# Performance work log

Hardware: AMD Instinct MI355X
Metric: run time of the kernel (lower is better)

The kernel has to match this reference:

```python
import jax, jax.numpy as jnp
import numpy as np

C = 64
RED = 4            # attention reduction: conv_match C -> C//RED
CR = C // RED      # 16, also MultiScaleSpatialAttention reduced channels
N_HASHES = 4
CHUNK = 512
RES_SCALE = 0.1
EPS = 5e-5


def conv2d(x, w, b=None, padding=0, groups=1):
    out = jax.lax.conv_general_dilated(
        x, w, (1, 1), [(padding, padding), (padding, padding)],
        dimension_numbers=('NCHW', 'OIHW', 'NCHW'), feature_group_count=groups)
    if b is not None:
        out = out + b[None, :, None, None]
    return out


def ds_conv(x, pw_w, dw_w, dw_b, padding):
    # pointwise (no bias) then depthwise (bias)
    x = conv2d(x, pw_w)
    return conv2d(x, dw_w, dw_b, padding=padding, groups=dw_w.shape[0])


def pool2(x, mode):
    B, Cc, H, W = x.shape
    xr = x.reshape(B, Cc, H // 2, 2, W // 2, 2)
    return xr.max(axis=(3, 5)) if mode == 'max' else xr.mean(axis=(3, 5))


def bilinear_ac(x, out_h, out_w):
    # bilinear interpolation with align_corners=True (matches F.interpolate)
    B, Cc, h, w = x.shape
    def coords(n_in, n_out):
        pos = jnp.arange(n_out, dtype=x.dtype) * ((n_in - 1) / (n_out - 1))
        lo = jnp.floor(pos).astype(jnp.int32)
        hi = jnp.minimum(lo + 1, n_in - 1)
        frac = pos - lo.astype(x.dtype)
        return lo, hi, frac
    lo_h, hi_h, fh = coords(h, out_h)
    x = x[:, :, lo_h, :] * (1 - fh)[None, None, :, None] + x[:, :, hi_h, :] * fh[None, None, :, None]
    lo_w, hi_w, fw = coords(w, out_w)
    x = x[:, :, :, lo_w] * (1 - fw) + x[:, :, :, hi_w] * fw
    return x


def sparse_attn(x, wm, bm, wa, ba, rot):
    # NLSN-style LSH-chunked non-local sparse attention
    N, Cc, H, W = x.shape
    L = H * W
    xe = conv2d(x, wm, bm).reshape(N, -1, L).transpose(0, 2, 1)   # [N,L,Ce]
    ye = conv2d(x, wa, ba).reshape(N, -1, L).transpose(0, 2, 1)   # [N,L,C]
    Ce = xe.shape[-1]
    n_chunks = L // CHUNK                     # L multiple of CHUNK here -> no padding
    buckets = min(n_chunks + n_chunks % 2, 128)
    # LSH hashing (rot: [Ce, n_hashes, buckets//2])
    rv = jnp.einsum('blf,fhi->bhli', xe, rot)
    rv = jnp.concatenate([rv, -rv], axis=-1)  # [N,nh,L,buckets]
    codes = jnp.argmax(rv, axis=-1) + (jnp.arange(N_HASHES) * buckets)[None, :, None]
    codes = codes.reshape(N, -1)              # [N, nh*L]
    idx = jnp.argsort(codes, axis=-1)
    undo = jnp.argsort(idx, axis=-1)
    mod_idx = idx % L
    xs = jnp.take_along_axis(xe, mod_idx[:, :, None], axis=1)     # [N,nh*L,Ce]
    ys = jnp.take_along_axis(ye, mod_idx[:, :, None], axis=1)     # [N,nh*L,C]
    xb = xs.reshape(N, N_HASHES, n_chunks, CHUNK, Ce)
    yb = ys.reshape(N, N_HASHES, n_chunks, CHUNK, Cc)
    xm = xb / jnp.maximum(jnp.linalg.norm(xb, axis=-1, keepdims=True), EPS)
    def adj(t):  # add previous / next bucket (circular)
        return jnp.concatenate([t, jnp.roll(t, 1, axis=2), jnp.roll(t, -1, axis=2)], axis=3)
    xm3, yb3 = adj(xm), adj(yb)
    raw = jnp.einsum('bhkie,bhkje->bhkij', xb, xm3)               # [N,nh,k,CHUNK,3*CHUNK]
    bscore = jax.nn.logsumexp(raw, axis=-1, keepdims=True)
    score = jnp.exp(raw - bscore)
    ret = jnp.einsum('bhkij,bhkje->bhkie', score, yb3)            # [N,nh,k,CHUNK,C]
    ret = ret.reshape(N, N_HASHES * L, Cc)
    bscore = bscore.reshape(N, N_HASHES * L)
    ret = jnp.take_along_axis(ret, undo[:, :, None], axis=1).reshape(N, N_HASHES, L, Cc)
    bscore = jnp.take_along_axis(bscore, undo, axis=1).reshape(N, N_HASHES, L, 1)
    probs = jax.nn.softmax(bscore, axis=1)                        # over hash rounds
    out = (ret * probs).sum(axis=1)                               # [N,L,C]
    out = out.transpose(0, 2, 1).reshape(N, Cc, H, W)
    return out * RES_SCALE + x


def setup_inputs() -> dict:
    key = jax.random.key(0)
    ks = iter(jax.random.split(key, 40))
    w = lambda *s: jax.random.normal(next(ks), s, jnp.float32) * 0.1
    inp = {
        'x': jax.random.normal(next(ks), (2, C, 128, 128), jnp.float32),
        'spa_down_w': w(CR, C, 1, 1), 'spa_down_b': w(CR),
        's0_pw_w': w(2 * CR, CR, 1, 1), 's0_dw_w': w(2 * CR, 1, 1, 1), 's0_dw_b': w(2 * CR),
        'br3_pw_w': w(CR, CR, 1, 1), 'br3_dw_w': w(CR, 1, 3, 3), 'br3_dw_b': w(CR),
        'br5_pw_w': w(CR, CR, 1, 1), 'br5_dw_w': w(CR, 1, 5, 5), 'br5_dw_b': w(CR),
        'br7_pw_w': w(CR, CR, 1, 1), 'br7_dw_w': w(CR, 1, 7, 7), 'br7_dw_b': w(CR),
        'fusion_w': w(C, 8 * CR, 1, 1), 'fusion_b': w(C),
        'resid_w': w(C, C, 1, 1), 'resid_b': w(C),
        'ca_w1': w(C // 16, C, 1, 1), 'ca_b1': w(C // 16),
        'ca_w2': w(C, C // 16, 1, 1), 'ca_b2': w(C),
        'conv1x1_w': w(C, C, 1, 1), 'conv1x1_b': w(C),
        'match_w': w(CR, C, 1, 1), 'match_b': w(CR),
        'asm_w': w(C, C, 1, 1), 'asm_b': w(C),
        'rot': jax.random.normal(next(ks), (CR, N_HASHES, 16), jnp.float32),  # buckets//2 = 16
        'collect_w': w(C, C, 1, 1), 'collect_b': w(C),
    }
    return inp


def reference(x, spa_down_w, spa_down_b, s0_pw_w, s0_dw_w, s0_dw_b,
              br3_pw_w, br3_dw_w, br3_dw_b, br5_pw_w, br5_dw_w, br5_dw_b,
              br7_pw_w, br7_dw_w, br7_dw_b, fusion_w, fusion_b,
              resid_w, resid_b, ca_w1, ca_b1, ca_w2, ca_b2,
              conv1x1_w, conv1x1_b, match_w, match_b, asm_w, asm_b, rot,
              collect_w, collect_b):
    B, Cc, H, W = x.shape
    # --- MultiScaleSpatialAttention ---
    xr = conv2d(x, spa_down_w, spa_down_b)                # [B,16,H,W]
    s0 = ds_conv(xr, s0_pw_w, s0_dw_w, s0_dw_b, padding=0)
    feats = [s0]
    for pw, dw, db, pad in ((br3_pw_w, br3_dw_w, br3_dw_b, 1),
                            (br5_pw_w, br5_dw_w, br5_dw_b, 2),
                            (br7_pw_w, br7_dw_w, br7_dw_b, 3)):
        mx = ds_conv(pool2(xr, 'max'), pw, dw, db, pad)
        av = ds_conv(pool2(xr, 'avg'), pw, dw, db, pad)
        feats.append(jnp.concatenate([bilinear_ac(mx, H, W), bilinear_ac(av, H, W)], axis=1))
    attn = jax.nn.sigmoid(conv2d(jnp.concatenate(feats, axis=1), fusion_w, fusion_b))
    spa_mask = x * attn + conv2d(x, resid_w, resid_b)
    # --- CALayer ---
    y = x.mean(axis=(2, 3), keepdims=True)
    y = jax.nn.sigmoid(conv2d(jax.nn.relu(conv2d(y, ca_w1, ca_b1)), ca_w2, ca_b2))
    spe_mask = x * y
    # --- combine + SparseMaskConv (n_layers=1: attention then 1x1 collect) ---
    mask = conv2d(spa_mask + spe_mask, conv1x1_w, conv1x1_b) + x
    fea = sparse_attn(mask, match_w, match_b, asm_w, asm_b, rot)
    out1 = conv2d(fea, collect_w, collect_b)
    return out1 + x
```

## Files before the change

### kernel.cpp

```cpp
#include <hip/hip_runtime.h>
#include <math.h>

static constexpr int NB = 2;
static constexpr int NC = 64;
static constexpr int NHp = 128, NWp = 128;
static constexpr int NL = NHp * NWp;
static constexpr int NCR = 16;
static constexpr int NL2 = 64 * 64;
static constexpr int NHASH = 4;
static constexpr int CHUNKSZ = 512;
static constexpr int NCHUNKS = 32;
static constexpr int TOT = NHASH * NL;
static constexpr int NKEY = 128;
static constexpr int NTILE = 256;
static constexpr int TILESZ = TOT / NTILE;

typedef _Float16 half4 __attribute__((ext_vector_type(4)));
typedef _Float16 half8 __attribute__((ext_vector_type(8)));
typedef float f32x4 __attribute__((ext_vector_type(4)));

static constexpr size_t OFF_MASK = 0;
static constexpr size_t OFF_FEA  = OFF_MASK + (size_t)NB*NC*NL;
static constexpr size_t OFF_XE   = OFF_FEA  + (size_t)NB*NC*NL;
static constexpr size_t OFF_XEH  = OFF_XE   + (size_t)NB*NL*NCR;
static constexpr size_t OFF_XENH = OFF_XEH  + (size_t)NB*NL*NCR/2;
static constexpr size_t OFF_YEH  = OFF_XENH + (size_t)NB*NL*NCR/2;
static constexpr size_t OFF_RET  = OFF_YEH  + (size_t)NB*NL*NC/2;
static constexpr size_t OFF_BSC  = OFF_RET  + (size_t)NB*TOT*NC/2;
static constexpr size_t OFF_INT  = OFF_BSC  + (size_t)NB*TOT;
static constexpr size_t IOFF_CODES = 0;
static constexpr size_t IOFF_IDX   = IOFF_CODES + (size_t)NB*TOT;
static constexpr size_t IOFF_UNDO  = IOFF_IDX   + (size_t)NB*TOT;
static constexpr size_t IOFF_HIST  = IOFF_UNDO  + (size_t)NB*TOT;
static constexpr size_t IOFF_OFFS  = IOFF_HIST  + (size_t)NB*NKEY*NTILE/2;
static constexpr size_t IOFF_END   = IOFF_OFFS  + (size_t)NB*NKEY*NTILE/2;
static constexpr size_t OFF_CAY = OFF_INT + IOFF_END;
static constexpr size_t OFF_CAS = OFF_CAY + 128;
static constexpr size_t OFF_CRW = OFF_CAS + 128;
static constexpr size_t OFF_CRB = OFF_CRW + 4096;
static constexpr size_t OFF_PMX   = OFF_FEA;
static constexpr size_t OFF_PAV   = OFF_PMX  + (size_t)NB*NCR*NL2;
static constexpr size_t OFF_PTMP  = OFF_PAV  + (size_t)NB*NCR*NL2;
static constexpr size_t OFF_DWT   = OFF_PTMP + (size_t)6*NB*NCR*NL2;
static_assert(OFF_DWT + (size_t)6*NB*NCR*NL2 <= OFF_XE, "halfres overlay fits");
static constexpr size_t OFF_XR    = OFF_XE;
static constexpr size_t OFF_FEATS = OFF_XR + (size_t)NB*NCR*NL;
static_assert(OFF_FEATS + (size_t)NB*128*NL <= OFF_BSC, "feats overlay fits");
static constexpr size_t OFF_PRE1  = OFF_FEA;

__device__ __forceinline__ float sigmoidf_(float v){ return 1.0f/(1.0f + expf(-v)); }


__global__ __launch_bounds__(256,4) void k_xr(const float* __restrict__ x,
                     const float* __restrict__ w,
                     const float* __restrict__ b, float* __restrict__ xr){
  int gid = blockIdx.x*256 + threadIdx.x;
  int pix = gid >> 1, hf = gid & 1;
  int bb = pix >> 14, p = pix & (NL-1);
  const float* xi = x + (size_t)bb*NC*NL + (size_t)hf*32*NL + p;
  float acc[16];
  #pragma unroll
  for (int oc=0; oc<16; ++oc) acc[oc] = hf ? 0.f : b[oc];
  for (int ic0=0; ic0<32; ic0+=16){
    float r[16];
    #pragma unroll
    for (int j=0; j<16; ++j) r[j] = xi[(size_t)(ic0+j)*NL];
    #pragma unroll
    for (int oc=0; oc<16; ++oc){
      #pragma unroll
      for (int j=0; j<16; ++j) acc[oc] += r[j]*w[oc*64 + hf*32 + ic0 + j];
    }
  }
  #pragma unroll
  for (int oc=0; oc<16; ++oc) acc[oc] += __shfl_xor(acc[oc], 1, 64);
  if (!hf){
    float* xo = xr + (size_t)bb*NCR*NL + p;
    #pragma unroll
    for (int oc=0; oc<16; ++oc) xo[(size_t)oc*NL] = acc[oc];
  }
}

__global__ __launch_bounds__(256,4) void k_s0(const float* __restrict__ xr,
                     const float* __restrict__ pw,
                     const float* __restrict__ dww, const float* __restrict__ dwb,
                     float* __restrict__ feats){
  int gid = blockIdx.x*256 + threadIdx.x;
  int oc0 = blockIdx.y*16;
  int bb = gid >> 14, p = gid & (NL-1);
  const float* xi = xr + (size_t)bb*NCR*NL + p;
  float r[16];
  #pragma unroll
  for (int ic=0; ic<16; ++ic) r[ic] = xi[(size_t)ic*NL];
  float* fo = feats + (size_t)bb*128*NL + p;
  #pragma unroll
  for (int j=0; j<16; ++j){
    int oc = oc0 + j;
    float s = 0.f;
    #pragma unroll
    for (int ic=0; ic<16; ++ic) s += r[ic]*pw[oc*16+ic];
    fo[(size_t)oc*NL] = s*dww[oc] + dwb[oc];
  }
}

__global__ void k_pool(const float* __restrict__ xr, float* __restrict__ pmax,
                       float* __restrict__ pavg){
  int gid = blockIdx.x*256 + threadIdx.x;
  if (gid >= NB*NCR*NL2) return;
  int p = gid & (NL2-1); int t = gid >> 12; int c = t & 15; int bb = t >> 4;
  int y = p >> 6, x2 = p & 63;
  const float* base = xr + (size_t)(bb*NCR + c)*NL + (size_t)(2*y)*NWp + 2*x2;
  float a = base[0], b_ = base[1], c_ = base[NWp], d = base[NWp+1];
  pmax[gid] = fmaxf(fmaxf(a,b_), fmaxf(c_,d));
  pavg[gid] = 0.25f*(a+b_+c_+d);
}

__global__ void k_pw16_all(const float* __restrict__ pmx, const float* __restrict__ pav,
                           const float* __restrict__ w0, const float* __restrict__ w1,
                           const float* __restrict__ w2, float* __restrict__ out){
  int gid = blockIdx.x*256 + threadIdx.x;
  if (gid >= 6*NB*NL2) return;
  int p = gid & (NL2-1); int t = gid >> 12; int bb = t & 1; int combo = t >> 1;
  int br = combo >> 1, mode = combo & 1;
  const float* w = (br==0) ? w0 : (br==1) ? w1 : w2;
  const float* in = ((mode==0) ? pmx : pav) + (size_t)bb*NCR*NL2 + p;
  float r[16];
  #pragma unroll
  for (int ic=0; ic<16; ++ic) r[ic] = in[(size_t)ic*NL2];
  float* oo = out + ((size_t)(combo*NB + bb)*NCR)*NL2 + p;
  #pragma unroll
  for (int oc=0; oc<16; ++oc){
    float s = 0.f;
    #pragma unroll
    for (int ic=0; ic<16; ++ic) s += r[ic]*w[oc*16+ic];
    oo[(size_t)oc*NL2] = s;
  }
}

__global__ void k_dw_all(const float* __restrict__ in,
                         const float* __restrict__ w3, const float* __restrict__ b3,
                         const float* __restrict__ w5, const float* __restrict__ b5,
                         const float* __restrict__ w7, const float* __restrict__ b7,
                         float* __restrict__ out){
  int gid = blockIdx.x*256 + threadIdx.x;
  if (gid >= 6*NB*NCR*NL2) return;
  int p = gid & (NL2-1); int t = gid >> 12; int c = t & 15; int r2 = t >> 4;
  int bb = r2 & 1; int combo = r2 >> 1;
  int br = combo >> 1;
  int K = (br==0) ? 3 : (br==1) ? 5 : 7; int P = K >> 1;
  const float* w = (br==0) ? w3 : (br==1) ? w5 : w7;
  const float* bias = (br==0) ? b3 : (br==1) ? b5 : b7;
  int y = p >> 6, x = p & 63;
  const float* xi = in + ((size_t)(combo*NB + bb)*NCR + c)*NL2;
  float s = bias[c];
  for (int dy=0; dy<K; ++dy){
    int iy = y + dy - P;
    if ((unsigned)iy < 64u){
      for (int dx=0; dx<K; ++dx){
        int ix = x + dx - P;
        if ((unsigned)ix < 64u) s += xi[iy*64 + ix] * w[(c*K + dy)*K + dx];
      }
    }
  }
  out[gid] = s;
}

__global__ void k_up_all(const float* __restrict__ in, float* __restrict__ feats){
  int gid = blockIdx.x*256 + threadIdx.x;
  if (gid >= 6*NB*NCR*NL) return;
  int p = gid & (NL-1); int t = gid >> 14; int c = t & 15; int r2 = t >> 4;
  int bb = r2 & 1; int combo = r2 >> 1;
  int y = p >> 7, x = p & 127;
  const float sc = 63.0f/127.0f;
  float fy = y*sc; int ly = (int)floorf(fy); int hy = min(ly+1, 63); fy -= (float)ly;
  float fx = x*sc; int lx = (int)floorf(fx); int hx = min(lx+1, 63); float gx = fx - (float)lx;
  const float* xi = in + ((size_t)(combo*NB + bb)*NCR + c)*NL2;
  float v0 = xi[ly*64+lx]*(1.f-fy) + xi[hy*64+lx]*fy;
  float v1 = xi[ly*64+hx]*(1.f-fy) + xi[hy*64+hx]*fy;
  int coff = 32 + combo*16 + c;
  feats[(size_t)bb*128*NL + (size_t)coff*NL + p] = v0*(1.f-gx) + v1*gx;
}

__global__ void k_camean(const float* __restrict__ x, float* __restrict__ cay){
  __shared__ float red[256];
  int bc = blockIdx.x; int tid = threadIdx.x;
  float s = 0.f;
  for (int i = tid; i < NL; i += 256) s += x[(size_t)bc*NL + i];
  red[tid] = s; __syncthreads();
  for (int st=128; st>0; st>>=1){ if (tid<st) red[tid]+=red[tid+st]; __syncthreads(); }
  if (tid==0) cay[bc] = red[0] / (float)NL;
}

__global__ void k_camlp(const float* __restrict__ cay,
                        const float* __restrict__ w1, const float* __restrict__ b1,
                        const float* __restrict__ w2, const float* __restrict__ b2,
                        float* __restrict__ cas){
  __shared__ float z[NB*4];
  int tid = threadIdx.x;
  if (tid < NB*4){
    int bb = tid >> 2, j = tid & 3;
    float s = b1[j];
    for (int ic=0; ic<NC; ++ic) s += cay[bb*NC+ic]*w1[j*NC+ic];
    z[tid] = fmaxf(s, 0.f);
  }
  __syncthreads();
  if (tid < NB*NC){
    int bb = tid >> 6, oc = tid & 63;
    float s = b2[oc];
    #pragma unroll
    for (int j=0; j<4; ++j) s += z[bb*4+j]*w2[oc*4+j];
    cas[tid] = sigmoidf_(s);
  }
}

__global__ void k_wprod(const float* __restrict__ c11w, const float* __restrict__ c11b,
                        const float* __restrict__ rw, const float* __restrict__ rb,
                        float* __restrict__ crw, float* __restrict__ crb){
  int gid = blockIdx.x*256 + threadIdx.x;
  if (gid >= 4096) return;
  int o = gid >> 6, i = gid & 63;
  float s = 0.f;
  for (int k=0; k<64; ++k) s += c11w[o*64+k]*rw[k*64+i];
  crw[gid] = s;
  if (i == 0){
    float t = c11b[o];
    for (int k=0; k<64; ++k) t += c11w[o*64+k]*rb[k];
    crb[o] = t;
  }
}

__global__ __launch_bounds__(256,4) void k_attnmul(const float* __restrict__ x,
                          const float* __restrict__ feats,
                          const float* __restrict__ fw, const float* __restrict__ fb,
                          const float* __restrict__ cas, float* __restrict__ pre1){
  int gid = blockIdx.x*256 + threadIdx.x;
  int oc0 = blockIdx.y*16;
  int bb = gid >> 14, p = gid & (NL-1);
  const float* fi = feats + (size_t)bb*128*NL + p;
  float acc[16];
  #pragma unroll
  for (int j=0; j<16; ++j) acc[j] = fb[oc0+j];
  for (int k0=0; k0<128; k0+=8){
    float fr[8];
    #pragma unroll
    for (int j=0; j<8; ++j) fr[j] = fi[(size_t)(k0+j)*NL];
    #pragma unroll
    for (int j=0; j<16; ++j){
      #pragma unroll
      for (int t=0; t<8; ++t) acc[j] += fr[t]*fw[(oc0+j)*128+k0+t];
    }
  }
  const float* xb = x + (size_t)bb*NC*NL + p;
  float* po = pre1 + (size_t)bb*NC*NL + p;
  #pragma unroll
  for (int j=0; j<16; ++j){
    int oc = oc0 + j;
    float xv = xb[(size_t)oc*NL];
    po[(size_t)oc*NL] = xv*(sigmoidf_(acc[j]) + cas[bb*64+oc]);
  }
}

__global__ __launch_bounds__(256,4) void k_mask(const float* __restrict__ pre1,
                       const float* __restrict__ c11w,
                       const float* __restrict__ crw, const float* __restrict__ crb,
                       const float* __restrict__ x, float* __restrict__ mask){
  int gid = blockIdx.x*256 + threadIdx.x;
  int oc0 = blockIdx.y*16;
  int bb = gid >> 14, p = gid & (NL-1);
  const float* pi = pre1 + (size_t)bb*NC*NL + p;
  const float* xi = x + (size_t)bb*NC*NL + p;
  float acc[16];
  #pragma unroll
  for (int j=0; j<16; ++j) acc[j] = crb[oc0+j];
  for (int ic0=0; ic0<64; ic0+=8){
    float pr[8], xr8[8];
    #pragma unroll
    for (int j=0; j<8; ++j){ pr[j] = pi[(size_t)(ic0+j)*NL]; xr8[j] = xi[(size_t)(ic0+j)*NL]; }
    #pragma unroll
    for (int j=0; j<16; ++j){
      #pragma unroll
      for (int t=0; t<8; ++t)
        acc[j] += pr[t]*c11w[(oc0+j)*64+ic0+t] + xr8[t]*crw[(oc0+j)*64+ic0+t];
    }
  }
  float* mo = mask + (size_t)bb*NC*NL + p;
  #pragma unroll
  for (int j=0; j<16; ++j){
    int oc = oc0 + j;
    mo[(size_t)oc*NL] = acc[j] + xi[(size_t)oc*NL];
  }
}


__global__ __launch_bounds__(256,4) void k_xe(const float* __restrict__ mask,
                     const float* __restrict__ w, const float* __restrict__ b,
                     const float* __restrict__ rot,
                     _Float16* __restrict__ xeh, _Float16* __restrict__ xenh,
                     int* __restrict__ codes){
  int gid = blockIdx.x*256 + threadIdx.x;
  int pix = gid >> 1, hf = gid & 1;
  int bb = pix >> 14, l = pix & (NL-1);
  const float* mi = mask + (size_t)bb*NC*NL + (size_t)hf*32*NL + l;
  float acc[16];
  #pragma unroll
  for (int oc=0; oc<16; ++oc) acc[oc] = hf ? 0.f : b[oc];
  for (int ic0=0; ic0<32; ic0+=16){
    float r[16];
    #pragma unroll
    for (int j=0; j<16; ++j) r[j] = mi[(size_t)(ic0+j)*NL];
    #pragma unroll
    for (int oc=0; oc<16; ++oc){
      #pragma unroll
      for (int j=0; j<16; ++j) acc[oc] += r[j]*w[oc*64 + hf*32 + ic0 + j];
    }
  }
  #pragma unroll
  for (int oc=0; oc<16; ++oc) acc[oc] += __shfl_xor(acc[oc], 1, 64);
  if (!hf){
    float n2 = 0.f;
    #pragma unroll
    for (int oc=0; oc<16; ++oc) n2 += acc[oc]*acc[oc];
    float inv = 1.0f / fmaxf(sqrtf(n2), 5e-5f);
    _Float16* ho = xeh + (size_t)pix*NCR;
    _Float16* no = xenh + (size_t)pix*NCR;
    #pragma unroll
    for (int g=0; g<4; ++g){
      half4 hv, nv;
      #pragma unroll
      for (int j=0; j<4; ++j){ hv[j] = (_Float16)acc[g*4+j]; nv[j] = (_Float16)(acc[g*4+j]*inv); }
      *(half4*)(ho + g*4) = hv;
      *(half4*)(no + g*4) = nv;
    }
  }
  #pragma unroll
  for (int hh=0; hh<2; ++hh){
    int h = hf*2 + hh;
    float rv[16];
    #pragma unroll
    for (int i=0; i<16; ++i){
      float s = 0.f;
      #pragma unroll
      for (int f=0; f<16; ++f) s += acc[f]*rot[(f*NHASH + h)*16 + i];
      rv[i] = s;
    }
    float best = -1e30f; int bi = 0;
    #pragma unroll
    for (int i=0; i<16; ++i){ if (rv[i] > best){ best = rv[i]; bi = i; } }
    #pragma unroll
    for (int i=0; i<16; ++i){ float val = -rv[i]; if (val > best){ best = val; bi = 16+i; } }
    codes[((bb*NHASH + h) << 14) + l] = bi + h*32;
  }
}

__global__ __launch_bounds__(256,4) void k_yeh(const float* __restrict__ mask,
                      const float* __restrict__ w,
                      const float* __restrict__ b, _Float16* __restrict__ yeh){
  int gid = blockIdx.x*256 + threadIdx.x;
  int oc0 = blockIdx.y*16;
  int bb = gid >> 14, l = gid & (NL-1);
  const float* mi = mask + (size_t)bb*NC*NL + l;
  float acc[16];
  #pragma unroll
  for (int j=0; j<16; ++j) acc[j] = b[oc0+j];
  for (int ic0=0; ic0<64; ic0+=8){
    float r[8];
    #pragma unroll
    for (int j=0; j<8; ++j) r[j] = mi[(size_t)(ic0+j)*NL];
    #pragma unroll
    for (int j=0; j<16; ++j){
      #pragma unroll
      for (int t=0; t<8; ++t) acc[j] += r[t]*w[(oc0+j)*64+ic0+t];
    }
  }
  _Float16* yo = yeh + (size_t)(bb*NL + l)*NC + oc0;
  #pragma unroll
  for (int g=0; g<2; ++g){
    half8 h;
    #pragma unroll
    for (int j=0; j<8; ++j) h[j] = (_Float16)acc[g*8+j];
    *(half8*)(yo + g*8) = h;
  }
}

__global__ void k_hist(const int* __restrict__ codes, int* __restrict__ hist){
  __shared__ int h[NKEY];
  int bt = blockIdx.x; int bb = bt >> 8; int tile = bt & 255;
  int tid = threadIdx.x;
  h[tid] = 0; __syncthreads();
  for (int i = tid; i < TILESZ; i += 128)
    atomicAdd(&h[codes[bb*TOT + tile*TILESZ + i]], 1);
  __syncthreads();
  hist[bb*NKEY*NTILE + tid*NTILE + tile] = h[tid];
}

__global__ void k_scan(const int* __restrict__ hist, int* __restrict__ offs){
  __shared__ int part[256];
  int bb = blockIdx.x; int t = threadIdx.x;
  const int* hi = hist + (size_t)bb*NKEY*NTILE;
  int* oo = offs + (size_t)bb*NKEY*NTILE;
  int s = 0;
  for (int i=0; i<128; ++i) s += hi[t*128 + i];
  part[t] = s; __syncthreads();
  if (t == 0){ int acc = 0; for (int i=0;i<256;++i){ int v=part[i]; part[i]=acc; acc+=v; } }
  __syncthreads();
  int run = part[t];
  for (int i=0; i<128; ++i){ int v = hi[t*128+i]; oo[t*128+i] = run; run += v; }
}

__global__ void k_scatter(const int* __restrict__ codes, const int* __restrict__ offs,
                          int* __restrict__ idx, int* __restrict__ undo){
  __shared__ int cnt[NKEY];
  int tid = threadIdx.x;
  cnt[tid] = 0; __syncthreads();
  if (tid == 0){
    int bt = blockIdx.x; int bb = bt >> 8; int tile = bt & 255;
    const int* cb = codes + bb*TOT;
    const int* ob = offs + (size_t)bb*NKEY*NTILE;
    int* ib = idx + bb*TOT;
    int* ub = undo + bb*TOT;
    #pragma unroll 4
    for (int i=0; i<TILESZ; ++i){
      int j = tile*TILESZ + i;
      int k = cb[j];
      int pos = ob[k*NTILE + tile] + cnt[k]++;
      ib[pos] = j;
      ub[j] = pos;
    }
  }
}

__global__ __launch_bounds__(512) void k_attn(
    const _Float16* __restrict__ xeh, const _Float16* __restrict__ xenh,
    const _Float16* __restrict__ yeh, const int* __restrict__ idx,
    _Float16* __restrict__ retb, float* __restrict__ bsc){
  __shared__ _Float16 kt[64*24];
  __shared__ _Float16 vt[64*72];
  int blk = blockIdx.x;
  int qh = blk & 1; int kk = (blk >> 1) & 31; int h = (blk >> 6) & 3; int bb = blk >> 8;
  int tid = threadIdx.x;
  int w = tid >> 6, lane = tid & 63, col = lane & 15, grp = lane >> 4;
  const int* idxb = idx + bb*TOT;
  int qbase = h*NL + kk*CHUNKSZ + qh*256 + w*32;

  half4 qfr[2]; int posq[2];
  #pragma unroll
  for (int qf=0; qf<2; ++qf){
    posq[qf] = qbase + qf*16 + col;
    int lq = idxb[posq[qf]] & (NL-1);
    qfr[qf] = *(const half4*)(xeh + ((size_t)bb*NL + lq)*16 + grp*4);
  }

  f32x4 O[4][2];
  #pragma unroll
  for (int a=0; a<4; ++a)
    #pragma unroll
    for (int b=0; b<2; ++b) O[a][b] = (f32x4){0.f,0.f,0.f,0.f};
  float m_[2] = {-1e30f,-1e30f};
  float ssum[2] = {0.f,0.f};

  for (int t=0; t<24; ++t){
    __syncthreads();
    {
      int kx = tid & 63, c0 = (tid >> 6) * 8;
      int jj = t*64 + kx; int sec = jj >> 9; int j0 = jj & 511;
      int cc = kk + ((sec==1) ? -1 : (sec==2) ? 1 : 0);
      cc = (cc + NCHUNKS) & (NCHUNKS-1);
      int lv = idxb[h*NL + cc*CHUNKSZ + j0] & (NL-1);
      half8 vv = *(const half8*)(yeh + ((size_t)bb*NL + lv)*64 + c0);
      #pragma unroll
      for (int j=0; j<8; ++j) vt[(c0+j)*72 + kx] = vv[j];
    }
    if (tid < 128){
      int r = tid >> 1, hf = tid & 1;
      int jj = t*64 + r; int sec = jj >> 9; int j0 = jj & 511;
      int cc = kk + ((sec==1) ? -1 : (sec==2) ? 1 : 0);
      cc = (cc + NCHUNKS) & (NCHUNKS-1);
      int lk = idxb[h*NL + cc*CHUNKSZ + j0] & (NL-1);
      *(half8*)(kt + r*24 + hf*8) =
          *(const half8*)(xenh + ((size_t)bb*NL + lk)*16 + hf*8);
    }
    __syncthreads();

    f32x4 S[4][2];
    #pragma unroll
    for (int kb=0; kb<4; ++kb){
      half4 ka = *(const half4*)(kt + (kb*16 + col)*24 + grp*4);
      #pragma unroll
      for (int qf=0; qf<2; ++qf)
        S[kb][qf] = __builtin_amdgcn_mfma_f32_16x16x16f16(
            ka, qfr[qf], (f32x4){0.f,0.f,0.f,0.f}, 0, 0, 0);
    }

    half4 pf[2][4];
    #pragma unroll
    for (int qf=0; qf<2; ++qf){
      float mt = -1e30f;
      #pragma unroll
      for (int kb=0; kb<4; ++kb)
        #pragma unroll
        for (int i=0; i<4; ++i) mt = fmaxf(mt, S[kb][qf][i]);
      mt = fmaxf(mt, __shfl_xor(mt, 16, 64));
      mt = fmaxf(mt, __shfl_xor(mt, 32, 64));
      if (__any(mt > m_[qf] + 8.0f)){
        float mn = fmaxf(m_[qf], mt);
        float sc = __expf(m_[qf] - mn);
        ssum[qf] *= sc;
        m_[qf] = mn;
        #pragma unroll
        for (int cf=0; cf<4; ++cf)
          #pragma unroll
          for (int i=0; i<4; ++i) O[cf][qf][i] *= sc;
      }
      float ps = 0.f;
      #pragma unroll
      for (int kb=0; kb<4; ++kb){
        #pragma unroll
        for (int i=0; i<4; ++i){
          float p = __expf(S[kb][qf][i] - m_[qf]);
          ps += p;
          pf[qf][kb][i] = (_Float16)p;
        }
      }
      ps += __shfl_xor(ps, 16, 64);
      ps += __shfl_xor(ps, 32, 64);
      ssum[qf] += ps;
    }

    #pragma unroll
    for (int cf=0; cf<4; ++cf){
      #pragma unroll
      for (int kb=0; kb<4; ++kb){
        half4 va = *(const half4*)(vt + (cf*16 + col)*72 + kb*16 + grp*4);
        #pragma unroll
        for (int qf=0; qf<2; ++qf)
          O[cf][qf] = __builtin_amdgcn_mfma_f32_16x16x16f16(
              va, pf[qf][kb], O[cf][qf], 0, 0, 0);
      }
    }
  }

  #pragma unroll
  for (int qf=0; qf<2; ++qf){
    float inv = 1.0f/ssum[qf];
    size_t rb = ((size_t)bb*TOT + posq[qf])*64;
    #pragma unroll
    for (int cf=0; cf<4; ++cf){
      half4 o;
      #pragma unroll
      for (int i=0; i<4; ++i) o[i] = (_Float16)(O[cf][qf][i]*inv);
      *(half4*)(retb + rb + cf*16 + grp*4) = o;
    }
    if (grp == 0) bsc[(size_t)bb*TOT + posq[qf]] = m_[qf] + logf(ssum[qf]);
  }
}

__global__ __launch_bounds__(256,4) void k_combine(const _Float16* __restrict__ retb,
                          const float* __restrict__ bsc,
                          const int* __restrict__ undo, const float* __restrict__ mask,
                          float* __restrict__ fea){
  int gid = blockIdx.x*256 + threadIdx.x;
  int c0 = blockIdx.y*32;
  int bb = gid >> 14; int l = gid & (NL-1);
  const int* ub = undo + bb*TOT;
  int pos[4]; float sc[4];
  #pragma unroll
  for (int h=0; h<4; ++h){ pos[h] = ub[h*NL + l]; sc[h] = bsc[bb*TOT + pos[h]]; }
  float mx = fmaxf(fmaxf(sc[0],sc[1]), fmaxf(sc[2],sc[3]));
  float e[4]; float tot = 0.f;
  #pragma unroll
  for (int h=0; h<4; ++h){ e[h] = __expf(sc[h]-mx); tot += e[h]; }
  float inv = 0.1f/tot;
  const float* mb_ = mask + (size_t)bb*NC*NL + l;
  float* fo = fea + (size_t)bb*NC*NL + l;
  const _Float16* r0 = retb + ((size_t)bb*TOT + pos[0])*NC + c0;
  const _Float16* r1 = retb + ((size_t)bb*TOT + pos[1])*NC + c0;
  const _Float16* r2 = retb + ((size_t)bb*TOT + pos[2])*NC + c0;
  const _Float16* r3 = retb + ((size_t)bb*TOT + pos[3])*NC + c0;
  #pragma unroll
  for (int g=0; g<4; ++g){
    half8 v0 = *(const half8*)(r0 + g*8);
    half8 v1 = *(const half8*)(r1 + g*8);
    half8 v2 = *(const half8*)(r2 + g*8);
    half8 v3 = *(const half8*)(r3 + g*8);
    #pragma unroll
    for (int j=0; j<8; ++j){
      int c = c0 + g*8 + j;
      float v = (float)v0[j]*e[0] + (float)v1[j]*e[1] + (float)v2[j]*e[2] + (float)v3[j]*e[3];
      fo[(size_t)c*NL] = v*inv + mb_[(size_t)c*NL];
    }
  }
}

__global__ __launch_bounds__(256,4) void k_collect(const float* __restrict__ fea,
                          const float* __restrict__ w,
                          const float* __restrict__ b, const float* __restrict__ x,
                          float* __restrict__ out){
  int gid = blockIdx.x*256 + threadIdx.x;
  int oc0 = blockIdx.y*16;
  int bb = gid >> 14, p = gid & (NL-1);
  const float* fi = fea + (size_t)bb*NC*NL + p;
  const float* xi = x + (size_t)bb*NC*NL + p;
  float acc[16];
  #pragma unroll
  for (int j=0; j<16; ++j) acc[j] = b[oc0+j];
  for (int ic0=0; ic0<64; ic0+=8){
    float r[8];
    #pragma unroll
    for (int j=0; j<8; ++j) r[j] = fi[(size_t)(ic0+j)*NL];
    #pragma unroll
    for (int j=0; j<16; ++j){
      #pragma unroll
      for (int t=0; t<8; ++t) acc[j] += r[t]*w[(oc0+j)*64+ic0+t];
    }
  }
  float* oo = out + (size_t)bb*NC*NL + p;
  #pragma unroll
  for (int j=0; j<16; ++j){
    int oc = oc0 + j;
    oo[(size_t)oc*NL] = acc[j] + xi[(size_t)oc*NL];
  }
}

extern "C" void kernel_launch(void* const* d_in, const int* in_sizes, int n_in,
                              void* d_out, int out_size, void* d_ws, size_t ws_size,
                              hipStream_t stream) {
  const float* x        = (const float*)d_in[0];
  const float* spa_dw   = (const float*)d_in[1];
  const float* spa_db   = (const float*)d_in[2];
  const float* s0_pw    = (const float*)d_in[3];
  const float* s0_dww   = (const float*)d_in[4];
  const float* s0_dwb   = (const float*)d_in[5];
  const float* fus_w    = (const float*)d_in[15];
  const float* fus_b    = (const float*)d_in[16];
  const float* res_w    = (const float*)d_in[17];
  const float* res_b    = (const float*)d_in[18];
  const float* ca_w1    = (const float*)d_in[19];
  const float* ca_b1    = (const float*)d_in[20];
  const float* ca_w2    = (const float*)d_in[21];
  const float* ca_b2    = (const float*)d_in[22];
  const float* c11_w    = (const float*)d_in[23];
  const float* c11_b    = (const float*)d_in[24];
  const float* match_w  = (const float*)d_in[25];
  const float* match_b  = (const float*)d_in[26];
  const float* asm_w    = (const float*)d_in[27];
  const float* asm_b    = (const float*)d_in[28];
  const float* rot      = (const float*)d_in[29];
  const float* col_w    = (const float*)d_in[30];
  const float* col_b    = (const float*)d_in[31];
  float* out = (float*)d_out;

  float* ws    = (float*)d_ws;
  float* mask  = ws + OFF_MASK;
  float* fea   = ws + OFF_FEA;
  _Float16* xeh  = (_Float16*)(ws + OFF_XEH);
  _Float16* xenh = (_Float16*)(ws + OFF_XENH);
  _Float16* yeh  = (_Float16*)(ws + OFF_YEH);
  _Float16* retb = (_Float16*)(ws + OFF_RET);
  float* bsc   = ws + OFF_BSC;
  int*   ib    = (int*)(ws + OFF_INT);
  int* codes   = ib + IOFF_CODES;
  int* idx     = ib + IOFF_IDX;
  int* undo    = ib + IOFF_UNDO;
  int* hist    = ib + IOFF_HIST;
  int* offs    = ib + IOFF_OFFS;
  float* cay   = ws + OFF_CAY;
  float* cas   = ws + OFF_CAS;
  float* crw   = ws + OFF_CRW;
  float* crb   = ws + OFF_CRB;
  float* xr    = ws + OFF_XR;
  float* feats = ws + OFF_FEATS;
  float* pmx   = ws + OFF_PMX;
  float* pav   = ws + OFF_PAV;
  float* ptmp  = ws + OFF_PTMP;
  float* dwt   = ws + OFF_DWT;
  float* pre1  = ws + OFF_PRE1;

  k_xr<<<(NB*NL*2)/256, 256, 0, stream>>>(x, spa_dw, spa_db, xr);
  k_wprod<<<16, 256, 0, stream>>>(c11_w, c11_b, res_w, res_b, crw, crb);
  k_s0<<<dim3((NB*NL)/256, 2), 256, 0, stream>>>(xr, s0_pw, s0_dww, s0_dwb, feats);
  k_pool<<<(NB*NCR*NL2)/256, 256, 0, stream>>>(xr, pmx, pav);
  k_pw16_all<<<(6*NB*NL2)/256, 256, 0, stream>>>(pmx, pav,
      (const float*)d_in[6], (const float*)d_in[9], (const float*)d_in[12], ptmp);
  k_dw_all<<<(6*NB*NCR*NL2)/256, 256, 0, stream>>>(ptmp,
      (const float*)d_in[7], (const float*)d_in[8],
      (const float*)d_in[10], (const float*)d_in[11],
      (const float*)d_in[13], (const float*)d_in[14], dwt);
  k_up_all<<<(6*NB*NCR*NL)/256, 256, 0, stream>>>(dwt, feats);
  k_camean<<<NB*NC, 256, 0, stream>>>(x, cay);
  k_camlp<<<1, 128, 0, stream>>>(cay, ca_w1, ca_b1, ca_w2, ca_b2, cas);
  k_attnmul<<<dim3((NB*NL)/256, 4), 256, 0, stream>>>(x, feats, fus_w, fus_b, cas, pre1);
  k_mask<<<dim3((NB*NL)/256, 4), 256, 0, stream>>>(pre1, c11_w, crw, crb, x, mask);

  k_xe<<<(NB*NL*2)/256, 256, 0, stream>>>(mask, match_w, match_b, rot, xeh, xenh, codes);
  k_yeh<<<dim3((NB*NL)/256, 4), 256, 0, stream>>>(mask, asm_w, asm_b, yeh);
  k_hist<<<NB*NTILE, 128, 0, stream>>>(codes, hist);
  k_scan<<<NB, 256, 0, stream>>>(hist, offs);
  k_scatter<<<NB*NTILE, 128, 0, stream>>>(codes, offs, idx, undo);
  k_attn<<<NB*NHASH*NCHUNKS*2, 512, 0, stream>>>(xeh, xenh, yeh, idx, retb, bsc);
  k_combine<<<dim3((NB*NL)/256, 2), 256, 0, stream>>>(retb, bsc, undo, mask, fea);
  k_collect<<<dim3((NB*NL)/256, 4), 256, 0, stream>>>(fea, col_w, col_b, x, out);
}
```

Measured before the change: 327.1 us.

## Fuse attnmul+mask and combine+collect, fold histogram into hashing, warp-parallel scatter

Merges the fusion-conv/attention-multiply kernel with the mask conv, keeping pre1 in shared memory, and merges the softmax combine with the collect conv, keeping fea in shared memory. This removes two full-resolution global round trips and two launches. The code histogram moves into k_xe through global atomics after a memset, which drops the separate k_hist pass. The serial single-thread scatter becomes a wave-parallel ballot-based ranking, k_yeh stages its inputs through LDS, and the vt LDS pitch changes. The global atomics may contend, and the per-wave cnt updates rely on ordering within a wave.

```diff
diff --git a/kernel.cpp b/kernel.cpp
--- a/kernel.cpp
+++ b/kernel.cpp
@@ -46,7 +46,6 @@
 static constexpr size_t OFF_XR    = OFF_XE;
 static constexpr size_t OFF_FEATS = OFF_XR + (size_t)NB*NCR*NL;
 static_assert(OFF_FEATS + (size_t)NB*128*NL <= OFF_BSC, "feats overlay fits");
-static constexpr size_t OFF_PRE1  = OFF_FEA;
 
 __device__ __forceinline__ float sigmoidf_(float v){ return 1.0f/(1.0f + expf(-v)); }
 
@@ -228,65 +227,71 @@
   }
 }
 
-__global__ __launch_bounds__(256,4) void k_attnmul(const float* __restrict__ x,
-                          const float* __restrict__ feats,
-                          const float* __restrict__ fw, const float* __restrict__ fb,
-                          const float* __restrict__ cas, float* __restrict__ pre1){
-  int gid = blockIdx.x*256 + threadIdx.x;
-  int oc0 = blockIdx.y*16;
-  int bb = gid >> 14, p = gid & (NL-1);
-  const float* fi = feats + (size_t)bb*128*NL + p;
-  float acc[16];
-  #pragma unroll
-  for (int j=0; j<16; ++j) acc[j] = fb[oc0+j];
-  for (int k0=0; k0<128; k0+=8){
-    float fr[8];
-    #pragma unroll
-    for (int j=0; j<8; ++j) fr[j] = fi[(size_t)(k0+j)*NL];
+__global__ __launch_bounds__(256) void k_fam(const float* __restrict__ x,
+                      const float* __restrict__ feats,
+                      const float* __restrict__ fw, const float* __restrict__ fb,
+                      const float* __restrict__ cas,
+                      const float* __restrict__ c11w,
+                      const float* __restrict__ crw, const float* __restrict__ crb,
+                      float* __restrict__ mask){
+  __shared__ float feats_s[128][64];
+  __shared__ float pre1_s[64][64];
+  int blk = blockIdx.x;
+  int bb = blk >> 8; int px0 = (blk & 255)*64;
+  int tid = threadIdx.x;
+  for (int i = tid; i < 128*64; i += 256){
+    int k = i >> 6, p = i & 63;
+    feats_s[k][p] = feats[(size_t)bb*128*NL + (size_t)k*NL + px0 + p];
+  }
+  __syncthreads();
+  int px = tid & 63, og = tid >> 6, oc0 = og*16;
+  const float* xb = x + (size_t)bb*NC*NL + px0 + px;
+  {
+    float acc[16];
+    #pragma unroll
+    for (int j=0; j<16; ++j) acc[j] = fb[oc0+j];
+    for (int k0=0; k0<128; k0+=8){
+      float fr[8];
+      #pragma unroll
+      for (int j=0; j<8; ++j) fr[j] = feats_s[k0+j][px];
+      #pragma unroll
+      for (int j=0; j<16; ++j){
+        #pragma unroll
+        for (int t=0; t<8; ++t) acc[j] += fr[t]*fw[(oc0+j)*128+k0+t];
+      }
+    }
     #pragma unroll
     for (int j=0; j<16; ++j){
-      #pragma unroll
-      for (int t=0; t<8; ++t) acc[j] += fr[t]*fw[(oc0+j)*128+k0+t];
-    }
-  }
-  const float* xb = x + (size_t)bb*NC*NL + p;
-  float* po = pre1 + (size_t)bb*NC*NL + p;
-  #pragma unroll
-  for (int j=0; j<16; ++j){
-    int oc = oc0 + j;
-    float xv = xb[(size_t)oc*NL];
-    po[(size_t)oc*NL] = xv*(sigmoidf_(acc[j]) + cas[bb*64+oc]);
-  }
-}
-
-__global__ __launch_bounds__(256,4) void k_mask(const float* __restrict__ pre1,
-                       const float* __restrict__ c11w,
-                       const float* __restrict__ crw, const float* __restrict__ crb,
-                       const float* __restrict__ x, float* __restrict__ mask){
-  int gid = blockIdx.x*256 + threadIdx.x;
-  int oc0 = blockIdx.y*16;
-  int bb = gid >> 14, p = gid & (NL-1);
-  const float* pi = pre1 + (size_t)bb*NC*NL + p;
-  const float* xi = x + (size_t)bb*NC*NL + p;
-  float acc[16];
-  #pragma unroll
-  for (int j=0; j<16; ++j) acc[j] = crb[oc0+j];
-  for (int ic0=0; ic0<64; ic0+=8){
-    float pr[8], xr8[8];
-    #pragma unroll
-    for (int j=0; j<8; ++j){ pr[j] = pi[(size_t)(ic0+j)*NL]; xr8[j] = xi[(size_t)(ic0+j)*NL]; }
+      int oc = oc0 + j;
+      float xv = xb[(size_t)oc*NL];
+      pre1_s[oc][px] = xv*(sigmoidf_(acc[j]) + cas[bb*64+oc]);
+    }
+  }
+  __syncthreads();
+  {
+    float acc[16];
+    #pragma unroll
+    for (int j=0; j<16; ++j) acc[j] = crb[oc0+j];
+    for (int ic0=0; ic0<64; ic0+=8){
+      float pr[8], xr8[8];
+      #pragma unroll
+      for (int j=0; j<8; ++j){
+        pr[j] = pre1_s[ic0+j][px];
+        xr8[j] = xb[(size_t)(ic0+j)*NL];
+      }
+      #pragma unroll
+      for (int j=0; j<16; ++j){
+        #pragma unroll
+        for (int t=0; t<8; ++t)
+          acc[j] += pr[t]*c11w[(oc0+j)*64+ic0+t] + xr8[t]*crw[(oc0+j)*64+ic0+t];
+      }
+    }
+    float* mo = mask + (size_t)bb*NC*NL + px0 + px;
     #pragma unroll
     for (int j=0; j<16; ++j){
-      #pragma unroll
-      for (int t=0; t<8; ++t)
-        acc[j] += pr[t]*c11w[(oc0+j)*64+ic0+t] + xr8[t]*crw[(oc0+j)*64+ic0+t];
-    }
-  }
-  float* mo = mask + (size_t)bb*NC*NL + p;
-  #pragma unroll
-  for (int j=0; j<16; ++j){
-    int oc = oc0 + j;
-    mo[(size_t)oc*NL] = acc[j] + xi[(size_t)oc*NL];
+      int oc = oc0 + j;
+      mo[(size_t)oc*NL] = acc[j] + xb[(size_t)oc*NL];
+    }
   }
 }
 
@@ -295,7 +300,7 @@
                      const float* __restrict__ w, const float* __restrict__ b,
                      const float* __restrict__ rot,
                      _Float16* __restrict__ xeh, _Float16* __restrict__ xenh,
-                     int* __restrict__ codes){
+                     int* __restrict__ codes, int* __restrict__ hist){
   int gid = blockIdx.x*256 + threadIdx.x;
   int pix = gid >> 1, hf = gid & 1;
   int bb = pix >> 14, l = pix & (NL-1);
@@ -347,31 +352,40 @@
     for (int i=0; i<16; ++i){ if (rv[i] > best){ best = rv[i]; bi = i; } }
     #pragma unroll
     for (int i=0; i<16; ++i){ float val = -rv[i]; if (val > best){ best = val; bi = 16+i; } }
-    codes[((bb*NHASH + h) << 14) + l] = bi + h*32;
-  }
-}
-
-__global__ __launch_bounds__(256,4) void k_yeh(const float* __restrict__ mask,
+    int code = bi + h*32;
+    codes[((bb*NHASH + h) << 14) + l] = code;
+    int tile = h*64 + (l >> 8);
+    atomicAdd(&hist[bb*NKEY*NTILE + code*NTILE + tile], 1);
+  }
+}
+
+__global__ __launch_bounds__(256) void k_yeh(const float* __restrict__ mask,
                       const float* __restrict__ w,
                       const float* __restrict__ b, _Float16* __restrict__ yeh){
-  int gid = blockIdx.x*256 + threadIdx.x;
-  int oc0 = blockIdx.y*16;
-  int bb = gid >> 14, l = gid & (NL-1);
-  const float* mi = mask + (size_t)bb*NC*NL + l;
+  __shared__ float m_s[64][64];
+  int blk = blockIdx.x;
+  int bb = blk >> 8; int px0 = (blk & 255)*64;
+  int tid = threadIdx.x;
+  for (int i = tid; i < 64*64; i += 256){
+    int c = i >> 6, p = i & 63;
+    m_s[c][p] = mask[(size_t)bb*NC*NL + (size_t)c*NL + px0 + p];
+  }
+  __syncthreads();
+  int px = tid & 63, og = tid >> 6, oc0 = og*16;
   float acc[16];
   #pragma unroll
   for (int j=0; j<16; ++j) acc[j] = b[oc0+j];
   for (int ic0=0; ic0<64; ic0+=8){
     float r[8];
     #pragma unroll
-    for (int j=0; j<8; ++j) r[j] = mi[(size_t)(ic0+j)*NL];
+    for (int j=0; j<8; ++j) r[j] = m_s[ic0+j][px];
     #pragma unroll
     for (int j=0; j<16; ++j){
       #pragma unroll
       for (int t=0; t<8; ++t) acc[j] += r[t]*w[(oc0+j)*64+ic0+t];
     }
   }
-  _Float16* yo = yeh + (size_t)(bb*NL + l)*NC + oc0;
+  _Float16* yo = yeh + (size_t)(bb*NL + px0 + px)*NC + oc0;
   #pragma unroll
   for (int g=0; g<2; ++g){
     half8 h;
@@ -379,17 +393,6 @@
     for (int j=0; j<8; ++j) h[j] = (_Float16)acc[g*8+j];
     *(half8*)(yo + g*8) = h;
   }
-}
-
-__global__ void k_hist(const int* __restrict__ codes, int* __restrict__ hist){
-  __shared__ int h[NKEY];
-  int bt = blockIdx.x; int bb = bt >> 8; int tile = bt & 255;
-  int tid = threadIdx.x;
-  h[tid] = 0; __syncthreads();
-  for (int i = tid; i < TILESZ; i += 128)
-    atomicAdd(&h[codes[bb*TOT + tile*TILESZ + i]], 1);
-  __syncthreads();
-  hist[bb*NKEY*NTILE + tid*NTILE + tile] = h[tid];
 }
 
 __global__ void k_scan(const int* __restrict__ hist, int* __restrict__ offs){
@@ -406,25 +409,40 @@
   for (int i=0; i<128; ++i){ int v = hi[t*128+i]; oo[t*128+i] = run; run += v; }
 }
 
-__global__ void k_scatter(const int* __restrict__ codes, const int* __restrict__ offs,
+__global__ __launch_bounds__(256) void k_scatter(const int* __restrict__ codes,
+                          const int* __restrict__ offs,
                           int* __restrict__ idx, int* __restrict__ undo){
-  __shared__ int cnt[NKEY];
-  int tid = threadIdx.x;
-  cnt[tid] = 0; __syncthreads();
-  if (tid == 0){
-    int bt = blockIdx.x; int bb = bt >> 8; int tile = bt & 255;
-    const int* cb = codes + bb*TOT;
-    const int* ob = offs + (size_t)bb*NKEY*NTILE;
-    int* ib = idx + bb*TOT;
-    int* ub = undo + bb*TOT;
-    #pragma unroll 4
-    for (int i=0; i<TILESZ; ++i){
-      int j = tile*TILESZ + i;
-      int k = cb[j];
-      int pos = ob[k*NTILE + tile] + cnt[k]++;
-      ib[pos] = j;
-      ub[j] = pos;
-    }
+  __shared__ int cnt[4][NKEY];
+  int wid = threadIdx.x >> 6, lane = threadIdx.x & 63;
+  int t4 = blockIdx.x;
+  int bb = t4 >> 6;
+  int tile = (t4 & 63)*4 + wid;
+  cnt[wid][lane] = 0; cnt[wid][64+lane] = 0;
+  const int* cb = codes + bb*TOT;
+  const int* ob = offs + (size_t)bb*NKEY*NTILE;
+  int* ib = idx + bb*TOT;
+  int* ub = undo + bb*TOT;
+  for (int g=0; g<4; ++g){
+    int j = tile*TILESZ + g*64 + lane;
+    int k = cb[j];
+    unsigned long long m = ~0ull;
+    #pragma unroll
+    for (int bit=0; bit<7; ++bit){
+      unsigned long long bmask = __ballot((k >> bit) & 1);
+      m &= ((k >> bit) & 1) ? bmask : ~bmask;
+    }
+    int rank = __popcll(m & ((1ull << lane) - 1ull));
+    int leader = __ffsll((unsigned long long)m) - 1;
+    int base = 0;
+    if (lane == leader){
+      base = cnt[wid][k];
+      cnt[wid][k] = base + __popcll(m);
+    }
+    base = __shfl(base, leader, 64);
+    int pos = ob[k*NTILE + tile] + base + rank;
+    ib[pos] = j;
+    ub[j] = pos;
+    __threadfence_block();
   }
 }
 
@@ -433,7 +451,7 @@
     const _Float16* __restrict__ yeh, const int* __restrict__ idx,
     _Float16* __restrict__ retb, float* __restrict__ bsc){
   __shared__ _Float16 kt[64*24];
-  __shared__ _Float16 vt[64*72];
+  __shared__ _Float16 vt[64*70];
   int blk = blockIdx.x;
   int qh = blk & 1; int kk = (blk >> 1) & 31; int h = (blk >> 6) & 3; int bb = blk >> 8;
   int tid = threadIdx.x;
@@ -467,7 +485,7 @@
       int lv = idxb[h*NL + cc*CHUNKSZ + j0] & (NL-1);
       half8 vv = *(const half8*)(yeh + ((size_t)bb*NL + lv)*64 + c0);
       #pragma unroll
-      for (int j=0; j<8; ++j) vt[(c0+j)*72 + kx] = vv[j];
+      for (int j=0; j<8; ++j) vt[(c0+j)*70 + kx] = vv[j];
     }
     if (tid < 128){
       int r = tid >> 1, hf = tid & 1;
@@ -529,7 +547,7 @@
     for (int cf=0; cf<4; ++cf){
       #pragma unroll
       for (int kb=0; kb<4; ++kb){
-        half4 va = *(const half4*)(vt + (cf*16 + col)*72 + kb*16 + grp*4);
+        half4 va = *(const half4*)(vt + (cf*16 + col)*70 + kb*16 + grp*4);
         #pragma unroll
         for (int qf=0; qf<2; ++qf)
           O[cf][qf] = __builtin_amdgcn_mfma_f32_16x16x16f16(
@@ -553,70 +571,69 @@
   }
 }
 
-__global__ __launch_bounds__(256,4) void k_combine(const _Float16* __restrict__ retb,
-                          const float* __restrict__ bsc,
-                          const int* __restrict__ undo, const float* __restrict__ mask,
-                          float* __restrict__ fea){
-  int gid = blockIdx.x*256 + threadIdx.x;
-  int c0 = blockIdx.y*32;
-  int bb = gid >> 14; int l = gid & (NL-1);
-  const int* ub = undo + bb*TOT;
-  int pos[4]; float sc[4];
-  #pragma unroll
-  for (int h=0; h<4; ++h){ pos[h] = ub[h*NL + l]; sc[h] = bsc[bb*TOT + pos[h]]; }
-  float mx = fmaxf(fmaxf(sc[0],sc[1]), fmaxf(sc[2],sc[3]));
-  float e[4]; float tot = 0.f;
-  #pragma unroll
-  for (int h=0; h<4; ++h){ e[h] = __expf(sc[h]-mx); tot += e[h]; }
-  float inv = 0.1f/tot;
-  const float* mb_ = mask + (size_t)bb*NC*NL + l;
-  float* fo = fea + (size_t)bb*NC*NL + l;
-  const _Float16* r0 = retb + ((size_t)bb*TOT + pos[0])*NC + c0;
-  const _Float16* r1 = retb + ((size_t)bb*TOT + pos[1])*NC + c0;
-  const _Float16* r2 = retb + ((size_t)bb*TOT + pos[2])*NC + c0;
-  const _Float16* r3 = retb + ((size_t)bb*TOT + pos[3])*NC + c0;
-  #pragma unroll
-  for (int g=0; g<4; ++g){
-    half8 v0 = *(const half8*)(r0 + g*8);
-    half8 v1 = *(const half8*)(r1 + g*8);
-    half8 v2 = *(const half8*)(r2 + g*8);
-    half8 v3 = *(const half8*)(r3 + g*8);
-    #pragma unroll
-    for (int j=0; j<8; ++j){
-      int c = c0 + g*8 + j;
-      float v = (float)v0[j]*e[0] + (float)v1[j]*e[1] + (float)v2[j]*e[2] + (float)v3[j]*e[3];
-      fo[(size_t)c*NL] = v*inv + mb_[(size_t)c*NL];
-    }
-  }
-}
-
-__global__ __launch_bounds__(256,4) void k_collect(const float* __restrict__ fea,
-                          const float* __restrict__ w,
-                          const float* __restrict__ b, const float* __restrict__ x,
-                          float* __restrict__ out){
-  int gid = blockIdx.x*256 + threadIdx.x;
-  int oc0 = blockIdx.y*16;
-  int bb = gid >> 14, p = gid & (NL-1);
-  const float* fi = fea + (size_t)bb*NC*NL + p;
-  const float* xi = x + (size_t)bb*NC*NL + p;
-  float acc[16];
-  #pragma unroll
-  for (int j=0; j<16; ++j) acc[j] = b[oc0+j];
-  for (int ic0=0; ic0<64; ic0+=8){
-    float r[8];
-    #pragma unroll
-    for (int j=0; j<8; ++j) r[j] = fi[(size_t)(ic0+j)*NL];
+__global__ __launch_bounds__(256) void k_fout(const _Float16* __restrict__ retb,
+                      const float* __restrict__ bsc,
+                      const int* __restrict__ undo, const float* __restrict__ mask,
+                      const float* __restrict__ w, const float* __restrict__ b,
+                      const float* __restrict__ x, float* __restrict__ out){
+  __shared__ float fea_s[64][64];
+  int blk = blockIdx.x;
+  int bb = blk >> 8; int px0 = (blk & 255)*64;
+  int tid = threadIdx.x;
+  int px = tid & 63, cg = tid >> 6;
+  int l = px0 + px;
+  {
+    const int* ub = undo + bb*TOT;
+    int pos[4]; float sc[4];
+    #pragma unroll
+    for (int h=0; h<4; ++h){ pos[h] = ub[h*NL + l]; sc[h] = bsc[bb*TOT + pos[h]]; }
+    float mx = fmaxf(fmaxf(sc[0],sc[1]), fmaxf(sc[2],sc[3]));
+    float e[4]; float tot = 0.f;
+    #pragma unroll
+    for (int h=0; h<4; ++h){ e[h] = __expf(sc[h]-mx); tot += e[h]; }
+    float inv = 0.1f/tot;
+    const float* mb_ = mask + (size_t)bb*NC*NL + l;
+    const _Float16* r0 = retb + ((size_t)bb*TOT + pos[0])*NC + cg*16;
+    const _Float16* r1 = retb + ((size_t)bb*TOT + pos[1])*NC + cg*16;
+    const _Float16* r2 = retb + ((size_t)bb*TOT + pos[2])*NC + cg*16;
+    const _Float16* r3 = retb + ((size_t)bb*TOT + pos[3])*NC + cg*16;
+    #pragma unroll
+    for (int g=0; g<2; ++g){
+      half8 v0 = *(const half8*)(r0 + g*8);
+      half8 v1 = *(const half8*)(r1 + g*8);
+      half8 v2 = *(const half8*)(r2 + g*8);
+      half8 v3 = *(const half8*)(r3 + g*8);
+      #pragma unroll
+      for (int j=0; j<8; ++j){
+        int c = cg*16 + g*8 + j;
+        float v = (float)v0[j]*e[0] + (float)v1[j]*e[1] + (float)v2[j]*e[2] + (float)v3[j]*e[3];
+        fea_s[c][px] = v*inv + mb_[(size_t)c*NL];
+      }
+    }
+  }
+  __syncthreads();
+  {
+    int oc0 = cg*16;
+    float acc[16];
+    #pragma unroll
+    for (int j=0; j<16; ++j) acc[j] = b[oc0+j];
+    for (int ic0=0; ic0<64; ic0+=8){
+      float r[8];
+      #pragma unroll
+      for (int j=0; j<8; ++j) r[j] = fea_s[ic0+j][px];
+      #pragma unroll
+      for (int j=0; j<16; ++j){
+        #pragma unroll
+        for (int t=0; t<8; ++t) acc[j] += r[t]*w[(oc0+j)*64+ic0+t];
+      }
+    }
+    const float* xi = x + (size_t)bb*NC*NL + l;
+    float* oo = out + (size_t)bb*NC*NL + l;
     #pragma unroll
     for (int j=0; j<16; ++j){
-      #pragma unroll
-      for (int t=0; t<8; ++t) acc[j] += r[t]*w[(oc0+j)*64+ic0+t];
-    }
-  }
-  float* oo = out + (size_t)bb*NC*NL + p;
-  #pragma unroll
-  for (int j=0; j<16; ++j){
-    int oc = oc0 + j;
-    oo[(size_t)oc*NL] = acc[j] + xi[(size_t)oc*NL];
+      int oc = oc0 + j;
+      oo[(size_t)oc*NL] = acc[j] + xi[(size_t)oc*NL];
+    }
   }
 }
 
@@ -650,7 +667,6 @@
 
   float* ws    = (float*)d_ws;
   float* mask  = ws + OFF_MASK;
-  float* fea   = ws + OFF_FEA;
   _Float16* xeh  = (_Float16*)(ws + OFF_XEH);
   _Float16* xenh = (_Float16*)(ws + OFF_XENH);
   _Float16* yeh  = (_Float16*)(ws + OFF_YEH);
@@ -672,7 +688,6 @@
   float* pav   = ws + OFF_PAV;
   float* ptmp  = ws + OFF_PTMP;
   float* dwt   = ws + OFF_DWT;
-  float* pre1  = ws + OFF_PRE1;
 
   k_xr<<<(NB*NL*2)/256, 256, 0, stream>>>(x, spa_dw, spa_db, xr);
   k_wprod<<<16, 256, 0, stream>>>(c11_w, c11_b, res_w, res_b, crw, crb);
@@ -687,15 +702,13 @@
   k_up_all<<<(6*NB*NCR*NL)/256, 256, 0, stream>>>(dwt, feats);
   k_camean<<<NB*NC, 256, 0, stream>>>(x, cay);
   k_camlp<<<1, 128, 0, stream>>>(cay, ca_w1, ca_b1, ca_w2, ca_b2, cas);
-  k_attnmul<<<dim3((NB*NL)/256, 4), 256, 0, stream>>>(x, feats, fus_w, fus_b, cas, pre1);
-  k_mask<<<dim3((NB*NL)/256, 4), 256, 0, stream>>>(pre1, c11_w, crw, crb, x, mask);
-
-  k_xe<<<(NB*NL*2)/256, 256, 0, stream>>>(mask, match_w, match_b, rot, xeh, xenh, codes);
-  k_yeh<<<dim3((NB*NL)/256, 4), 256, 0, stream>>>(mask, asm_w, asm_b, yeh);
-  k_hist<<<NB*NTILE, 128, 0, stream>>>(codes, hist);
+  k_fam<<<NB*NL/64, 256, 0, stream>>>(x, feats, fus_w, fus_b, cas, c11_w, crw, crb, mask);
+
+  hipMemsetAsync(hist, 0, (size_t)NB*NKEY*NTILE*sizeof(int), stream);
+  k_xe<<<(NB*NL*2)/256, 256, 0, stream>>>(mask, match_w, match_b, rot, xeh, xenh, codes, hist);
+  k_yeh<<<NB*NL/64, 256, 0, stream>>>(mask, asm_w, asm_b, yeh);
   k_scan<<<NB, 256, 0, stream>>>(hist, offs);
-  k_scatter<<<NB*NTILE, 128, 0, stream>>>(codes, offs, idx, undo);
+  k_scatter<<<NB*NTILE/4, 256, 0, stream>>>(codes, offs, idx, undo);
   k_attn<<<NB*NHASH*NCHUNKS*2, 512, 0, stream>>>(xeh, xenh, yeh, idx, retb, bsc);
-  k_combine<<<dim3((NB*NL)/256, 2), 256, 0, stream>>>(retb, bsc, undo, mask, fea);
-  k_collect<<<dim3((NB*NL)/256, 4), 256, 0, stream>>>(fea, col_w, col_b, x, out);
-}
+  k_fout<<<NB*NL/64, 256, 0, stream>>>(retb, bsc, undo, mask, col_w, col_b, x, out);
+}
```

After: 349.3 us. +6.8%, slower.
